# Optimization experiments

Measured on AMD Instinct MI355X. Metric: run time of the kernel, lower is better.

Reference implementation:

```python
import jax, jax.numpy as jnp
import numpy as np

N = 10000          # nodes
E_RAND = 320000    # random edges (avg degree 32)
F_IN = 512         # nfeat
HID = 256          # args.hid
HEADS = 8          # args.head
FH = HID // HEADS  # 32 per head
NCLASS = 40
TAU = 0.5
LAMDA = 0.5
K = 2


def setup_inputs() -> dict:
    key = jax.random.key(0)
    ks = jax.random.split(key, 16)
    # edge list: random edges + self-loops (so every dst segment is non-empty)
    src = jnp.concatenate([jax.random.randint(ks[0], (E_RAND,), 0, N), jnp.arange(N)])
    dst = jnp.concatenate([jax.random.randint(ks[1], (E_RAND,), 0, N), jnp.arange(N)])
    s = 0.05  # small init scale keeps exp() in attention/bind_loss stable
    return {
        "x": jax.random.normal(ks[2], (N, F_IN), jnp.float32),
        "src": src, "dst": dst,
        "W0": jax.random.normal(ks[3], (F_IN, HEADS, FH), jnp.float32) * s,
        "a0s": jax.random.normal(ks[4], (HEADS, FH), jnp.float32) * s,
        "a0d": jax.random.normal(ks[5], (HEADS, FH), jnp.float32) * s,
        "W1": jax.random.normal(ks[6], (HID, HEADS, FH), jnp.float32) * s,
        "a1s": jax.random.normal(ks[7], (HEADS, FH), jnp.float32) * s,
        "a1d": jax.random.normal(ks[8], (HEADS, FH), jnp.float32) * s,
        "W2": jax.random.normal(ks[9], (HID, HEADS, FH), jnp.float32) * s,
        "a2s": jax.random.normal(ks[10], (HEADS, FH), jnp.float32) * s,
        "a2d": jax.random.normal(ks[11], (HEADS, FH), jnp.float32) * s,
        "Wout": jax.random.normal(ks[12], (HID, HEADS, NCLASS), jnp.float32) * s,
        "aos": jax.random.normal(ks[13], (HEADS, NCLASS), jnp.float32) * s,
        "aod": jax.random.normal(ks[14], (HEADS, NCLASS), jnp.float32) * s,
    }


def _gat_layer(x, W, a_s, a_d, src, dst):
    """Sparse multi-head GAT layer: gather -> edge softmax -> scatter."""
    n = x.shape[0]
    h = jnp.einsum('nf,fhd->nhd', x, W)              # [N,H,Fh]
    es = jnp.sum(h * a_s, axis=-1)                    # [N,H]
    ed = jnp.sum(h * a_d, axis=-1)                    # [N,H]
    e = jax.nn.leaky_relu(es[src] + ed[dst], 0.2)     # [E,H]
    m = jax.ops.segment_max(e, dst, num_segments=n)   # per-dst max (stable softmax)
    w = jnp.exp(e - m[dst])
    z = jax.ops.segment_sum(w, dst, num_segments=n)
    alpha = w / z[dst]                                # [E,H]
    return jax.ops.segment_sum(alpha[:, :, None] * h[src], dst, num_segments=n)  # [N,H,Fh]


def _bind_loss(z):
    # z1 == z2 == z in the original call site: refl_sim == between_sim
    zn = z / jnp.maximum(jnp.linalg.norm(z, axis=1, keepdims=True), 1e-12)
    S = jnp.exp(jnp.matmul(zn, zn.T) / TAU)           # [N,N]
    d = jnp.diagonal(S)
    off = jnp.sum(S, axis=1) - d                      # masked (off-diagonal) row sum
    CT = -jnp.log(d / (off + off))                    # neg_c2.sum + neg_c3.sum
    return jnp.mean(CT)


def reference(x, src, dst, W0, a0s, a0d, W1, a1s, a1d, W2, a2s, a2d, Wout, aos, aod):
    layers = [(W0, a0s, a0d), (W1, a1s, a1d), (W2, a2s, a2d)]
    last = x
    loss = jnp.float32(0.0)
    for i, (W, as_, ad_) in enumerate(layers):
        cur = jax.nn.elu(_gat_layer(last, W, as_, ad_, src, dst))
        cur = cur.reshape(cur.shape[0], -1)           # concat heads -> [N, HID]
        if i > 0:
            beta = LAMDA / (i + 2)                    # MaskLayer(last, cur, lamda, i+2)
            cur = beta * last + (1.0 - beta) * cur
            if i % K == 0:
                loss = loss + _bind_loss(cur)
        last = cur
    out = _gat_layer(last, Wout, aos, aod, src, dst).mean(axis=1)  # avg heads -> [N,C]
    return (jax.nn.log_softmax(out, axis=1), loss)
```

## Files before the change

kernel.cpp:

```cpp
#include <hip/hip_runtime.h>
#include <hip/hip_bf16.h>
#include <math.h>

#define NN_F_IN   512
#define NN_HID    256
#define NN_HEADS  8
#define NN_FH     32
#define NN_NCLASS 40
#define TAU_F     0.5f
#define LAMDA_F   0.5f
#define ZN_SCALE  1.6986436f

typedef __attribute__((ext_vector_type(8))) short bf16x8;
typedef __attribute__((ext_vector_type(4))) float f32x4;

typedef __attribute__((address_space(1))) unsigned int gu32_t;
typedef __attribute__((address_space(3))) unsigned int lu32_t;

static __device__ __forceinline__ float lrelu02(float x) { return x >= 0.f ? x : 0.2f * x; }
static __device__ __forceinline__ float elu1(float x)    { return x > 0.f ? x : expm1f(x); }
static __device__ __forceinline__ float b2f(unsigned short u) {
    unsigned int x = ((unsigned int)u) << 16;
    return __uint_as_float(x);
}
static __device__ __forceinline__ unsigned short f2b(float f) {
    __hip_bfloat16 hb = __float2bfloat16(f);
    return *reinterpret_cast<unsigned short*>(&hb);
}

__global__ void prep_kernel(const float* __restrict__ x,
                            const float* __restrict__ W0, const float* __restrict__ W1,
                            const float* __restrict__ W2, const float* __restrict__ Wo,
                            unsigned short* __restrict__ Xb,
                            unsigned short* __restrict__ Wt0, unsigned short* __restrict__ Wt1,
                            unsigned short* __restrict__ Wt2, unsigned short* __restrict__ Wto,
                            int n4X) {
    int i = blockIdx.x * 256 + threadIdx.x;
    if (i < n4X) {
        float4 v = *(const float4*)(x + (size_t)i * 4);
        ushort4 o;
        o.x = f2b(v.x); o.y = f2b(v.y); o.z = f2b(v.z); o.w = f2b(v.w);
        *(ushort4*)(Xb + (size_t)i * 4) = o;
        return;
    }
    i -= n4X;
    if (i < 256 * 512) {
        int np = i >> 9, k = i & 511;
        Wt0[i] = f2b(W0[(size_t)k * 256 + np]);
        return;
    }
    i -= 256 * 512;
    if (i < 256 * 256) {
        int np = i >> 8, k = i & 255;
        Wt1[i] = f2b(W1[(size_t)k * 256 + np]);
        return;
    }
    i -= 256 * 256;
    if (i < 256 * 256) {
        int np = i >> 8, k = i & 255;
        Wt2[i] = f2b(W2[(size_t)k * 256 + np]);
        return;
    }
    i -= 256 * 256;
    if (i < 384 * 256) {
        int np = i >> 8, k = i & 255;
        Wto[i] = f2b(np < 320 ? Wo[(size_t)k * 320 + np] : 0.f);
    }
}

__global__ __launch_bounds__(256) void fc_mfma(const unsigned short* __restrict__ A,
                                               const unsigned short* __restrict__ B,
                                               unsigned short* __restrict__ H,
                                               int M, int K, int ncols, int ldH) {
    int t = threadIdx.x, lane = t & 63, wid = t >> 6;
    int wrow = wid >> 1, wcol = wid & 1;
    int l15 = lane & 15, lg = lane >> 4;
    int mbase = blockIdx.y * 64 + wrow * 32;
    int nbase = blockIdx.x * 64 + wcol * 32;

    const unsigned short* Ap[2];
    const unsigned short* Bp[2];
#pragma unroll
    for (int m = 0; m < 2; ++m) {
        int rr = mbase + m * 16 + l15;
        if (rr > M - 1) rr = M - 1;
        Ap[m] = A + (size_t)rr * K + lg * 8;
        Bp[m] = B + (size_t)(nbase + m * 16 + l15) * K + lg * 8;
    }
    f32x4 acc[2][2];
#pragma unroll
    for (int m = 0; m < 2; ++m)
#pragma unroll
        for (int nn = 0; nn < 2; ++nn)
#pragma unroll
            for (int r = 0; r < 4; ++r) acc[m][nn][r] = 0.f;

    bf16x8 aP[2], bP[2], aQ[2], bQ[2];
#pragma unroll
    for (int m = 0; m < 2; ++m) {
        aP[m] = *(const bf16x8*)(Ap[m]);
        bP[m] = *(const bf16x8*)(Bp[m]);
    }
    int nhalf = K >> 6;
    int kk = 32;
    for (int it = 0; it < nhalf; ++it) {
#pragma unroll
        for (int m = 0; m < 2; ++m) {
            aQ[m] = *(const bf16x8*)(Ap[m] + kk);
            bQ[m] = *(const bf16x8*)(Bp[m] + kk);
        }
#pragma unroll
        for (int m = 0; m < 2; ++m)
#pragma unroll
            for (int nn = 0; nn < 2; ++nn)
                acc[m][nn] = __builtin_amdgcn_mfma_f32_16x16x32_bf16(aP[m], bP[nn], acc[m][nn], 0, 0, 0);
        if (it + 1 < nhalf) {
#pragma unroll
            for (int m = 0; m < 2; ++m) {
                aP[m] = *(const bf16x8*)(Ap[m] + kk + 32);
                bP[m] = *(const bf16x8*)(Bp[m] + kk + 32);
            }
        }
#pragma unroll
        for (int m = 0; m < 2; ++m)
#pragma unroll
            for (int nn = 0; nn < 2; ++nn)
                acc[m][nn] = __builtin_amdgcn_mfma_f32_16x16x32_bf16(aQ[m], bQ[nn], acc[m][nn], 0, 0, 0);
        kk += 64;
    }
#pragma unroll
    for (int m = 0; m < 2; ++m) {
#pragma unroll
        for (int nn = 0; nn < 2; ++nn) {
            int col = nbase + nn * 16 + l15;
            if (col >= ncols) continue;
#pragma unroll
            for (int r = 0; r < 4; ++r) {
                int row = mbase + m * 16 + lg * 4 + r;
                if (row < M) H[(size_t)row * ldH + col] = f2b(acc[m][nn][r]);
            }
        }
    }
}

__global__ void attn_kernel(const unsigned short* __restrict__ Hm, const float* __restrict__ As,
                            const float* __restrict__ Ad, float* __restrict__ es,
                            float* __restrict__ ed, int n, int df) {
    int idx = blockIdx.x * blockDim.x + threadIdx.x;
    if (idx >= n * NN_HEADS) return;
    int nn = idx / NN_HEADS, hh = idx - nn * NN_HEADS;
    const unsigned short* hp = Hm + (size_t)nn * NN_HEADS * df + hh * df;
    const float* ap = As + hh * df;
    const float* bp = Ad + hh * df;
    float s1 = 0.f, s2 = 0.f;
    for (int d = 0; d < df; d += 4) {
        ushort4 hv = *(const ushort4*)(hp + d);
        float4 av = *(const float4*)(ap + d);
        float4 bv = *(const float4*)(bp + d);
        float h0 = b2f(hv.x), h1 = b2f(hv.y), h2 = b2f(hv.z), h3 = b2f(hv.w);
        s1 += h0 * av.x + h1 * av.y + h2 * av.z + h3 * av.w;
        s2 += h0 * bv.x + h1 * bv.y + h2 * bv.z + h3 * bv.w;
    }
    es[idx] = s1;
    ed[idx] = s2;
}

__global__ __launch_bounds__(256) void edge_wz(
    const float* __restrict__ es, const float* __restrict__ ed,
    const int* __restrict__ csr_src, const int* __restrict__ row_start,
    float* __restrict__ wC, float* __restrict__ zinv, int n) {
    int lane = threadIdx.x & 63;
    int nn   = blockIdx.x * 4 + (threadIdx.x >> 6);
    if (nn >= n) return;
    int s0 = row_start[nn], s1 = row_start[nn + 1];
    int h    = lane & 7;
    int slot = lane >> 3;
    float edh = ed[nn * NN_HEADS + h];
    float z = 0.f;
    for (int e = s0 + slot; e < s1; e += 8) {
        int sv = csr_src[e];
        float w = __expf(lrelu02(es[sv * NN_HEADS + h] + edh));
        wC[(size_t)e * NN_HEADS + h] = w;
        z += w;
    }
    z += __shfl_xor(z, 8, 64);
    z += __shfl_xor(z, 16, 64);
    z += __shfl_xor(z, 32, 64);
    if (slot == 0) zinv[nn * NN_HEADS + h] = 1.f / z;
}

__global__ void count_kernel(const int* __restrict__ dst, int* __restrict__ counts, int E) {
    int e = blockIdx.x * blockDim.x + threadIdx.x;
    if (e < E) atomicAdd(&counts[dst[e]], 1);
}

__global__ void scan_kernel(const int* __restrict__ counts, int* __restrict__ row_start,
                            int* __restrict__ cursor, int n) {
    __shared__ int s[1024];
    int t  = threadIdx.x;
    int ch = (n + 1023) / 1024;
    int lo = t * ch;
    int sum = 0;
    for (int j = 0; j < ch; ++j) {
        int i = lo + j;
        if (i < n) sum += counts[i];
    }
    s[t] = sum;
    __syncthreads();
    for (int off = 1; off < 1024; off <<= 1) {
        int v = 0;
        if (t >= off) v = s[t - off];
        __syncthreads();
        s[t] += v;
        __syncthreads();
    }
    int run = (t == 0) ? 0 : s[t - 1];
    for (int j = 0; j < ch; ++j) {
        int i = lo + j;
        if (i < n) {
            row_start[i] = run;
            cursor[i] = run;
            run += counts[i];
        }
    }
    if (t == 1023) row_start[n] = s[1023];
}

__global__ void scatter_kernel(const int* __restrict__ src, const int* __restrict__ dst,
                               int* __restrict__ cursor, int* __restrict__ csr_src, int E) {
    int e = blockIdx.x * blockDim.x + threadIdx.x;
    if (e < E) {
        int d   = dst[e];
        int pos = atomicAdd(&cursor[d], 1);
        csr_src[pos] = src[e];
    }
}

__global__ __launch_bounds__(256) void gather_hidden(
    const unsigned short* __restrict__ Hm, const float* __restrict__ es,
    const float* __restrict__ ed, const int* __restrict__ csr_src,
    const int* __restrict__ row_start, const unsigned short* __restrict__ last,
    unsigned short* __restrict__ out, int n, float beta) {
    int lane = threadIdx.x & 63;
    int nn   = blockIdx.x * 4 + (threadIdx.x >> 6);
    if (nn >= n) return;
    int s0 = row_start[nn], s1 = row_start[nn + 1];
    int h2 = lane >> 3;
    float edh = ed[nn * NN_HEADS + h2];

    float zacc = 0.f;
    float a0 = 0.f, a1 = 0.f, a2 = 0.f, a3 = 0.f;
    int fullEnd = s0 + ((s1 - s0) & ~7);
    int e = s0;
    for (; e < fullEnd; e += 8) {
        int idx[8];
        float q[8];
#pragma unroll
        for (int j = 0; j < 8; ++j) idx[j] = csr_src[e + j];
#pragma unroll
        for (int j = 0; j < 8; ++j) q[j] = es[idx[j] * NN_HEADS + h2];
        ushort4 r[8];
#pragma unroll
        for (int j = 0; j < 8; ++j) r[j] = *(const ushort4*)&Hm[(size_t)idx[j] * NN_HID + lane * 4];
#pragma unroll
        for (int j = 0; j < 8; ++j) {
            float w = __expf(lrelu02(q[j] + edh));
            zacc += w;
            a0 += w * b2f(r[j].x); a1 += w * b2f(r[j].y);
            a2 += w * b2f(r[j].z); a3 += w * b2f(r[j].w);
        }
    }
    if (e < s1) {
        int c = s1 - e;
        int idx[8];
        float q[8];
#pragma unroll
        for (int j = 0; j < 8; ++j) idx[j] = csr_src[(j < c) ? e + j : e];
#pragma unroll
        for (int j = 0; j < 8; ++j) q[j] = es[idx[j] * NN_HEADS + h2];
        ushort4 r[8];
#pragma unroll
        for (int j = 0; j < 8; ++j) r[j] = *(const ushort4*)&Hm[(size_t)idx[j] * NN_HID + lane * 4];
#pragma unroll
        for (int j = 0; j < 8; ++j) {
            if (j < c) {
                float w = __expf(lrelu02(q[j] + edh));
                zacc += w;
                a0 += w * b2f(r[j].x); a1 += w * b2f(r[j].y);
                a2 += w * b2f(r[j].z); a3 += w * b2f(r[j].w);
            }
        }
    }
    float zi = 1.f / zacc;
    float v0 = elu1(a0 * zi), v1 = elu1(a1 * zi), v2 = elu1(a2 * zi), v3 = elu1(a3 * zi);
    if (beta >= 0.f) {
        ushort4 lv = *(const ushort4*)&last[(size_t)nn * NN_HID + lane * 4];
        v0 = beta * b2f(lv.x) + (1.f - beta) * v0;
        v1 = beta * b2f(lv.y) + (1.f - beta) * v1;
        v2 = beta * b2f(lv.z) + (1.f - beta) * v2;
        v3 = beta * b2f(lv.w) + (1.f - beta) * v3;
    }
    ushort4 o;
    o.x = f2b(v0); o.y = f2b(v1); o.z = f2b(v2); o.w = f2b(v3);
    *(ushort4*)&out[(size_t)nn * NN_HID + lane * 4] = o;
}

__global__ void gather_final(const unsigned short* __restrict__ Hm, const float* __restrict__ wC,
                             const float* __restrict__ zinv, const int* __restrict__ csr_src,
                             const int* __restrict__ row_start, float* __restrict__ dout, int n) {
    int nn = blockIdx.x;
    __shared__ float accs[NN_HEADS * NN_NCLASS];
    int t = threadIdx.x;
    int s0 = row_start[nn], s1 = row_start[nn + 1];
    int hh = t / NN_NCLASS;
    float acc = 0.f;
    const int LD = NN_HEADS * NN_NCLASS;
    int fullEnd = s0 + ((s1 - s0) & ~7);
    int e = s0;
    for (; e < fullEnd; e += 8) {
        int idx[8];
        float wv[8];
#pragma unroll
        for (int j = 0; j < 8; ++j) {
            idx[j] = csr_src[e + j];
            wv[j]  = wC[(size_t)(e + j) * NN_HEADS + hh];
        }
        float v[8];
#pragma unroll
        for (int j = 0; j < 8; ++j) v[j] = b2f(Hm[(size_t)idx[j] * LD + t]);
#pragma unroll
        for (int j = 0; j < 8; ++j) acc += wv[j] * v[j];
    }
    if (e < s1) {
        int c = s1 - e;
        int idx[8];
        float wv[8];
#pragma unroll
        for (int j = 0; j < 8; ++j) {
            int p = (j < c) ? e + j : e;
            idx[j] = csr_src[p];
            wv[j]  = wC[(size_t)p * NN_HEADS + hh];
        }
        float v[8];
#pragma unroll
        for (int j = 0; j < 8; ++j) v[j] = b2f(Hm[(size_t)idx[j] * LD + t]);
#pragma unroll
        for (int j = 0; j < 8; ++j) {
            if (j < c) acc += wv[j] * v[j];
        }
    }
    accs[t] = acc * zinv[nn * NN_HEADS + hh];
    __syncthreads();
    if (t < 64) {
        float v = -INFINITY;
        if (t < NN_NCLASS) {
            float sacc = 0.f;
#pragma unroll
            for (int h2 = 0; h2 < NN_HEADS; ++h2) sacc += accs[h2 * NN_NCLASS + t];
            v = sacc * (1.f / NN_HEADS);
        }
        float mx = v;
#pragma unroll
        for (int o = 1; o < 64; o <<= 1) mx = fmaxf(mx, __shfl_xor(mx, o, 64));
        float ex = (t < NN_NCLASS) ? expf(v - mx) : 0.f;
        float se = ex;
#pragma unroll
        for (int o = 1; o < 64; o <<= 1) se += __shfl_xor(se, o, 64);
        if (t < NN_NCLASS) dout[(size_t)nn * NN_NCLASS + t] = (v - mx) - logf(se);
    }
}

__global__ void rownorm_kernel(const unsigned short* __restrict__ z, short* __restrict__ znb,
                               float* __restrict__ dvec, int n) {
    int nn = blockIdx.x;
    int t  = threadIdx.x;
    if (nn >= n) {
        znb[(size_t)nn * NN_HID + t] = 0;
        return;
    }
    float v  = b2f(z[(size_t)nn * NN_HID + t]);
    float sq = v * v;
#pragma unroll
    for (int o = 1; o < 64; o <<= 1) sq += __shfl_xor(sq, o, 64);
    __shared__ float ws[4];
    if ((t & 63) == 0) ws[t >> 6] = sq;
    __syncthreads();
    float s = ws[0] + ws[1] + ws[2] + ws[3];
    float m = fmaxf(sqrtf(s), 1e-12f);
    znb[(size_t)nn * NN_HID + t] = (short)f2b((v / m) * ZN_SCALE);
    if (t == 0) dvec[nn] = __expf((s / (m * m)) * (1.f / TAU_F));
}

__global__ __launch_bounds__(256) void gram_mfma(const short* __restrict__ znb,
                                                 float* __restrict__ P2d, int n,
                                                 int T, int nwg, int Npad) {
    __shared__ short As[128 * 32];
    __shared__ short Bs[128 * 32];

    int b = blockIdx.x;
    int q = nwg >> 3, r8 = nwg & 7, xc = b & 7, oo = b >> 3;
    int sid = (xc < r8 ? xc * (q + 1) : r8 * (q + 1) + (xc - r8) * q) + oo;
    int bi = 0, rem = sid;
    while (rem >= T - bi) { rem -= T - bi; ++bi; }
    int bj = bi + rem;
    int i0 = bi * 128, j0 = bj * 128;

    int t    = threadIdx.x;
    int lane = t & 63;
    int wid  = t >> 6;
    int wrow = wid >> 1, wcol = wid & 1;
    int l15  = lane & 15, lg = lane >> 4;

    int srow0 = 16 * (2 * wid + 0) + (lane >> 2);
    int srow1 = 16 * (2 * wid + 1) + (lane >> 2);
    int kc    = lane & 3;
    int kc0   = kc ^ ((srow0 >> 1) & 3);
    int kc1   = kc ^ ((srow1 >> 1) & 3);
    const short* gA0 = znb + (size_t)(i0 + srow0) * NN_HID + kc0 * 8;
    const short* gA1 = znb + (size_t)(i0 + srow1) * NN_HID + kc1 * 8;
    const short* gB0 = znb + (size_t)(j0 + srow0) * NN_HID + kc0 * 8;
    const short* gB1 = znb + (size_t)(j0 + srow1) * NN_HID + kc1 * 8;
    short* lA0 = As + (2 * wid + 0) * 512 + lane * 8;
    short* lA1 = As + (2 * wid + 1) * 512 + lane * 8;
    short* lB0 = Bs + (2 * wid + 0) * 512 + lane * 8;
    short* lB1 = Bs + (2 * wid + 1) * 512 + lane * 8;

    f32x4 acc[4][4];
#pragma unroll
    for (int m = 0; m < 4; ++m)
#pragma unroll
        for (int nn = 0; nn < 4; ++nn)
#pragma unroll
            for (int r = 0; r < 4; ++r) acc[m][nn][r] = 0.f;

#pragma unroll
    for (int s = 0; s < 8; ++s) {
        int ko = s * 32;
        __builtin_amdgcn_global_load_lds((gu32_t*)(gA0 + ko), (lu32_t*)lA0, 16, 0, 0);
        __builtin_amdgcn_global_load_lds((gu32_t*)(gA1 + ko), (lu32_t*)lA1, 16, 0, 0);
        __builtin_amdgcn_global_load_lds((gu32_t*)(gB0 + ko), (lu32_t*)lB0, 16, 0, 0);
        __builtin_amdgcn_global_load_lds((gu32_t*)(gB1 + ko), (lu32_t*)lB1, 16, 0, 0);
        __syncthreads();
        bf16x8 av[4], bv[4];
#pragma unroll
        for (int m = 0; m < 4; ++m) {
            int Ra = wrow * 64 + m * 16 + l15;
            int ca = lg ^ ((Ra >> 1) & 3);
            av[m] = *(const bf16x8*)&As[Ra * 32 + ca * 8];
        }
#pragma unroll
        for (int m = 0; m < 4; ++m) {
            int Rb = wcol * 64 + m * 16 + l15;
            int cb = lg ^ ((Rb >> 1) & 3);
            bv[m] = *(const bf16x8*)&Bs[Rb * 32 + cb * 8];
        }
#pragma unroll
        for (int m = 0; m < 4; ++m)
#pragma unroll
            for (int nn = 0; nn < 4; ++nn)
                acc[m][nn] = __builtin_amdgcn_mfma_f32_16x16x32_bf16(av[m], bv[nn], acc[m][nn], 0, 0, 0);
        __syncthreads();
    }

    int i0w = i0 + wrow * 64;
    int j0w = j0 + wcol * 64;
    bool diag = (bj == bi);
    if (bj == T - 1) {
#pragma unroll
        for (int m = 0; m < 4; ++m)
#pragma unroll
            for (int nn = 0; nn < 4; ++nn) {
                int gj = j0w + nn * 16 + l15;
                bool jok = gj < n;
#pragma unroll
                for (int r = 0; r < 4; ++r) {
                    int gi = i0w + m * 16 + lg * 4 + r;
                    acc[m][nn][r] = (jok && gi < n) ? __builtin_exp2f(acc[m][nn][r]) : 0.f;
                }
            }
    } else {
#pragma unroll
        for (int m = 0; m < 4; ++m)
#pragma unroll
            for (int nn = 0; nn < 4; ++nn)
#pragma unroll
                for (int r = 0; r < 4; ++r)
                    acc[m][nn][r] = __builtin_exp2f(acc[m][nn][r]);
    }
    float* rowslot = P2d + (size_t)(2 * bj + wcol) * Npad;
#pragma unroll
    for (int m = 0; m < 4; ++m) {
#pragma unroll
        for (int r = 0; r < 4; ++r) {
            float v = acc[m][0][r] + acc[m][1][r] + acc[m][2][r] + acc[m][3][r];
            v += __shfl_xor(v, 1, 64);
            v += __shfl_xor(v, 2, 64);
            v += __shfl_xor(v, 4, 64);
            v += __shfl_xor(v, 8, 64);
            if (l15 == 0) {
                int gi = i0w + m * 16 + lg * 4 + r;
                if (gi < n) rowslot[gi] = v;
            }
        }
    }
    if (!diag) {
        float* colslot = P2d + (size_t)(2 * bi + wrow) * Npad;
#pragma unroll
        for (int nn = 0; nn < 4; ++nn) {
            float v = 0.f;
#pragma unroll
            for (int m = 0; m < 4; ++m)
#pragma unroll
                for (int r = 0; r < 4; ++r) v += acc[m][nn][r];
            v += __shfl_xor(v, 16, 64);
            v += __shfl_xor(v, 32, 64);
            if (lg == 0) {
                int gj = j0w + nn * 16 + l15;
                if (gj < n) colslot[gj] = v;
            }
        }
    }
}

__global__ void fold_kernel(const float* __restrict__ P2d, float* __restrict__ R,
                            int n, int slots, int Npad) {
    int i = blockIdx.x * 256 + threadIdx.x;
    if (i >= n) return;
    const float* p = P2d + i;
    float s0 = 0.f, s1 = 0.f, s2 = 0.f, s3 = 0.f;
    int sl = 0;
    for (; sl + 4 <= slots; sl += 4) {
        s0 += p[(size_t)(sl + 0) * Npad];
        s1 += p[(size_t)(sl + 1) * Npad];
        s2 += p[(size_t)(sl + 2) * Npad];
        s3 += p[(size_t)(sl + 3) * Npad];
    }
    for (; sl < slots; ++sl) s0 += p[(size_t)sl * Npad];
    R[i] = (s0 + s1) + (s2 + s3);
}

__global__ void loss_kernel(const float* __restrict__ R, const float* __restrict__ dvec,
                            float* __restrict__ out_loss, int n) {
    __shared__ float s[1024];
    int t = threadIdx.x;
    float sum = 0.f;
    for (int i = t; i < n; i += 1024) {
        float d   = dvec[i];
        float off = R[i] - d;
        sum += -logf(d / (off + off));
    }
    s[t] = sum;
    __syncthreads();
    for (int o = 512; o > 0; o >>= 1) {
        if (t < o) s[t] += s[t + o];
        __syncthreads();
    }
    if (t == 0) *out_loss = s[0] / n;
}

extern "C" void kernel_launch(void* const* d_in, const int* in_sizes, int n_in,
                              void* d_out, int out_size, void* d_ws, size_t ws_size,
                              hipStream_t stream) {
    const float* x   = (const float*)d_in[0];
    const int*   src = (const int*)d_in[1];
    const int*   dst = (const int*)d_in[2];
    const float* W0  = (const float*)d_in[3];
    const float* a0s = (const float*)d_in[4];
    const float* a0d = (const float*)d_in[5];
    const float* W1  = (const float*)d_in[6];
    const float* a1s = (const float*)d_in[7];
    const float* a1d = (const float*)d_in[8];
    const float* W2  = (const float*)d_in[9];
    const float* a2s = (const float*)d_in[10];
    const float* a2d = (const float*)d_in[11];
    const float* Wout= (const float*)d_in[12];
    const float* aos = (const float*)d_in[13];
    const float* aod = (const float*)d_in[14];

    int N = in_sizes[0] / NN_F_IN;
    int E = in_sizes[1];
    int Npad = ((N + 127) / 128) * 128;
    int T = Npad / 128;
    int nwg = T * (T + 1) / 2;
    float* out = (float*)d_out;

    char*  ws  = (char*)d_ws;
    size_t off = 0;
    auto alloc = [&](size_t bytes) -> void* {
        void* p = ws + off;
        off += bytes;
        off = (off + 255) & ~(size_t)255;
        return p;
    };
    size_t hbBytes = (size_t)N * 320 * 2;
    size_t znBytes = (size_t)Npad * NN_HID * 2;
    unsigned short* Hb = (unsigned short*)alloc(hbBytes > znBytes ? hbBytes : znBytes);
    short* znb = (short*)Hb;
    unsigned short* Bl = (unsigned short*)alloc((size_t)N * NN_HID * 2);
    unsigned short* Bc = (unsigned short*)alloc((size_t)N * NN_HID * 2);
    size_t xbBytes = (size_t)N * NN_F_IN * 2;
    size_t p2Bytes = (size_t)2 * T * Npad * 4;
    void* XbP2d = alloc(xbBytes > p2Bytes ? xbBytes : p2Bytes);
    unsigned short* Xb  = (unsigned short*)XbP2d;
    float*          P2d = (float*)XbP2d;
    unsigned short* Wt0 = (unsigned short*)alloc((size_t)256 * 512 * 2);
    unsigned short* Wt1 = (unsigned short*)alloc((size_t)256 * 256 * 2);
    unsigned short* Wt2 = (unsigned short*)alloc((size_t)256 * 256 * 2);
    unsigned short* Wto = (unsigned short*)alloc((size_t)384 * 256 * 2);
    float* es     = (float*)alloc((size_t)N * NN_HEADS * 4);
    float* ed     = (float*)alloc((size_t)N * NN_HEADS * 4);
    float* wC     = (float*)alloc((size_t)E * NN_HEADS * 4);
    float* zinvA  = (float*)alloc((size_t)N * NN_HEADS * 4);
    float* Rrow   = (float*)alloc((size_t)N * 4);
    float* dvec   = (float*)alloc((size_t)N * 4);
    int*   counts = (int*)alloc((size_t)N * 4);
    int*   rs     = (int*)alloc((size_t)(N + 1) * 4);
    int*   cursor = (int*)alloc((size_t)N * 4);
    int*   csr    = (int*)alloc((size_t)E * 4);

    hipMemsetAsync(counts, 0, (size_t)N * 4, stream);
    count_kernel<<<(E + 255) / 256, 256, 0, stream>>>(dst, counts, E);
    scan_kernel<<<1, 1024, 0, stream>>>(counts, rs, cursor, N);
    scatter_kernel<<<(E + 255) / 256, 256, 0, stream>>>(src, dst, cursor, csr, E);

    int n4X = N * NN_F_IN / 4;
    int prepTotal = n4X + 256 * 512 + 256 * 256 + 256 * 256 + 384 * 256;
    prep_kernel<<<(prepTotal + 255) / 256, 256, 0, stream>>>(
        x, W0, W1, W2, Wout, Xb, Wt0, Wt1, Wt2, Wto, n4X);

    int atGrid = (N * NN_HEADS + 255) / 256;
    int ghGrid = (N + 3) / 4;
    int mT64 = (N + 63) / 64;

    fc_mfma<<<dim3(4, mT64), 256, 0, stream>>>(Xb, Wt0, Hb, N, 512, 256, 256);
    attn_kernel<<<atGrid, 256, 0, stream>>>(Hb, a0s, a0d, es, ed, N, NN_FH);
    gather_hidden<<<ghGrid, 256, 0, stream>>>(Hb, es, ed, csr, rs, nullptr, Bl, N, -1.f);

    fc_mfma<<<dim3(4, mT64), 256, 0, stream>>>(Bl, Wt1, Hb, N, 256, 256, 256);
    attn_kernel<<<atGrid, 256, 0, stream>>>(Hb, a1s, a1d, es, ed, N, NN_FH);
    gather_hidden<<<ghGrid, 256, 0, stream>>>(Hb, es, ed, csr, rs, Bl, Bc, N, LAMDA_F / 3.f);

    fc_mfma<<<dim3(4, mT64), 256, 0, stream>>>(Bc, Wt2, Hb, N, 256, 256, 256);
    attn_kernel<<<atGrid, 256, 0, stream>>>(Hb, a2s, a2d, es, ed, N, NN_FH);
    gather_hidden<<<ghGrid, 256, 0, stream>>>(Hb, es, ed, csr, rs, Bc, Bl, N, LAMDA_F / 4.f);

    rownorm_kernel<<<Npad, 256, 0, stream>>>(Bl, znb, dvec, N);
    gram_mfma<<<nwg, 256, 0, stream>>>(znb, P2d, N, T, nwg, Npad);
    fold_kernel<<<(N + 255) / 256, 256, 0, stream>>>(P2d, Rrow, N, 2 * T, Npad);
    loss_kernel<<<1, 1024, 0, stream>>>(Rrow, dvec, out + (size_t)N * NN_NCLASS, N);

    fc_mfma<<<dim3(5, mT64), 256, 0, stream>>>(Bl, Wto, Hb, N, 256, 320, 320);
    attn_kernel<<<atGrid, 256, 0, stream>>>(Hb, aos, aod, es, ed, N, NN_NCLASS);
    edge_wz<<<ghGrid, 256, 0, stream>>>(es, ed, csr, rs, wC, zinvA, N);
    gather_final<<<N, NN_HEADS * NN_NCLASS, 0, stream>>>(Hb, wC, zinvA, csr, rs, out, N);
}
```

Measured before the change: 384.8 us.

## Fuse attention scores into FC GEMM, row-norm into gather, double-buffer gram

Computes the per-head es/ed attention logits inside the FC MFMA epilogue using shuffles across the 32 columns of each head, which removes the three separate attn kernels for the hidden layers. The row normalisation for the contrastive loss moves into the last gather_hidden, removing the rownorm kernel, so znb gets its own buffer and its padding rows are zeroed by a memset. The gram kernel double-buffers its LDS tiles so the global-to-LDS load of the next K slice overlaps the MFMAs on the current one. The cost is extra LDS use and a separate znb allocation. The normalisation is now computed from fp32 values before bf16 rounding, so results can differ slightly.

```diff
diff --git a/kernel.cpp b/kernel.cpp
--- a/kernel.cpp
+++ b/kernel.cpp
@@ -65,6 +65,104 @@
     if (i < 384 * 256) {
         int np = i >> 8, k = i & 255;
         Wto[i] = f2b(np < 320 ? Wo[(size_t)k * 320 + np] : 0.f);
+    }
+}
+
+__global__ __launch_bounds__(256) void fc_attn_mfma(
+    const unsigned short* __restrict__ A, const unsigned short* __restrict__ B,
+    unsigned short* __restrict__ H, const float* __restrict__ As_,
+    const float* __restrict__ Ad_, float* __restrict__ es, float* __restrict__ ed,
+    int M, int K) {
+    const int ldH = 256;
+    int t = threadIdx.x, lane = t & 63, wid = t >> 6;
+    int wrow = wid >> 1, wcol = wid & 1;
+    int l15 = lane & 15, lg = lane >> 4;
+    int mbase = blockIdx.y * 64 + wrow * 32;
+    int nbase = blockIdx.x * 64 + wcol * 32;
+
+    const unsigned short* Ap[2];
+    const unsigned short* Bp[2];
+#pragma unroll
+    for (int m = 0; m < 2; ++m) {
+        int rr = mbase + m * 16 + l15;
+        if (rr > M - 1) rr = M - 1;
+        Ap[m] = A + (size_t)rr * K + lg * 8;
+        Bp[m] = B + (size_t)(nbase + m * 16 + l15) * K + lg * 8;
+    }
+    f32x4 acc[2][2];
+#pragma unroll
+    for (int m = 0; m < 2; ++m)
+#pragma unroll
+        for (int nn = 0; nn < 2; ++nn)
+#pragma unroll
+            for (int r = 0; r < 4; ++r) acc[m][nn][r] = 0.f;
+
+    bf16x8 aP[2], bP[2], aQ[2], bQ[2];
+#pragma unroll
+    for (int m = 0; m < 2; ++m) {
+        aP[m] = *(const bf16x8*)(Ap[m]);
+        bP[m] = *(const bf16x8*)(Bp[m]);
+    }
+    int nhalf = K >> 6;
+    int kk = 32;
+    for (int it = 0; it < nhalf; ++it) {
+#pragma unroll
+        for (int m = 0; m < 2; ++m) {
+            aQ[m] = *(const bf16x8*)(Ap[m] + kk);
+            bQ[m] = *(const bf16x8*)(Bp[m] + kk);
+        }
+#pragma unroll
+        for (int m = 0; m < 2; ++m)
+#pragma unroll
+            for (int nn = 0; nn < 2; ++nn)
+                acc[m][nn] = __builtin_amdgcn_mfma_f32_16x16x32_bf16(aP[m], bP[nn], acc[m][nn], 0, 0, 0);
+        if (it + 1 < nhalf) {
+#pragma unroll
+            for (int m = 0; m < 2; ++m) {
+                aP[m] = *(const bf16x8*)(Ap[m] + kk + 32);
+                bP[m] = *(const bf16x8*)(Bp[m] + kk + 32);
+            }
+        }
+#pragma unroll
+        for (int m = 0; m < 2; ++m)
+#pragma unroll
+            for (int nn = 0; nn < 2; ++nn)
+                acc[m][nn] = __builtin_amdgcn_mfma_f32_16x16x32_bf16(aQ[m], bQ[nn], acc[m][nn], 0, 0, 0);
+        kk += 64;
+    }
+#pragma unroll
+    for (int m = 0; m < 2; ++m) {
+#pragma unroll
+        for (int nn = 0; nn < 2; ++nn) {
+            int col = nbase + nn * 16 + l15;
+#pragma unroll
+            for (int r = 0; r < 4; ++r) {
+                int row = mbase + m * 16 + lg * 4 + r;
+                if (row < M) H[(size_t)row * ldH + col] = f2b(acc[m][nn][r]);
+            }
+        }
+    }
+    int hh = blockIdx.x * 2 + wcol;
+    float a0 = As_[hh * 32 + l15], a1 = As_[hh * 32 + 16 + l15];
+    float d0 = Ad_[hh * 32 + l15], d1 = Ad_[hh * 32 + 16 + l15];
+#pragma unroll
+    for (int m = 0; m < 2; ++m) {
+#pragma unroll
+        for (int r = 0; r < 4; ++r) {
+            float ps = acc[m][0][r] * a0 + acc[m][1][r] * a1;
+            float pd = acc[m][0][r] * d0 + acc[m][1][r] * d1;
+            ps += __shfl_xor(ps, 1, 64); pd += __shfl_xor(pd, 1, 64);
+            ps += __shfl_xor(ps, 2, 64); pd += __shfl_xor(pd, 2, 64);
+            ps += __shfl_xor(ps, 4, 64); pd += __shfl_xor(pd, 4, 64);
+            ps += __shfl_xor(ps, 8, 64); pd += __shfl_xor(pd, 8, 64);
+            if (l15 == 0) {
+                int row = mbase + m * 16 + lg * 4 + r;
+                if (row < M) {
+                    es[row * NN_HEADS + hh] = ps;
+                    ed[row * NN_HEADS + hh] = pd;
+                }
+            }
+        }
     }
 }
 
@@ -240,7 +338,8 @@
     const unsigned short* __restrict__ Hm, const float* __restrict__ es,
     const float* __restrict__ ed, const int* __restrict__ csr_src,
     const int* __restrict__ row_start, const unsigned short* __restrict__ last,
-    unsigned short* __restrict__ out, int n, float beta) {
+    unsigned short* __restrict__ out, int n, float beta,
+    unsigned short* __restrict__ znb, float* __restrict__ dvec) {
     int lane = threadIdx.x & 63;
     int nn   = blockIdx.x * 4 + (threadIdx.x >> 6);
     if (nn >= n) return;
@@ -303,6 +402,23 @@
     ushort4 o;
     o.x = f2b(v0); o.y = f2b(v1); o.z = f2b(v2); o.w = f2b(v3);
     *(ushort4*)&out[(size_t)nn * NN_HID + lane * 4] = o;
+
+    if (znb) {
+        float ss = v0 * v0 + v1 * v1 + v2 * v2 + v3 * v3;
+        ss += __shfl_xor(ss, 1, 64);
+        ss += __shfl_xor(ss, 2, 64);
+        ss += __shfl_xor(ss, 4, 64);
+        ss += __shfl_xor(ss, 8, 64);
+        ss += __shfl_xor(ss, 16, 64);
+        ss += __shfl_xor(ss, 32, 64);
+        float m = fmaxf(sqrtf(ss), 1e-12f);
+        float sc = ZN_SCALE / m;
+        ushort4 zo;
+        zo.x = f2b(v0 * sc); zo.y = f2b(v1 * sc);
+        zo.z = f2b(v2 * sc); zo.w = f2b(v3 * sc);
+        *(ushort4*)&znb[(size_t)nn * NN_HID + lane * 4] = zo;
+        if (lane == 0) dvec[nn] = __expf((ss / (m * m)) * (1.f / TAU_F));
+    }
 }
 
 __global__ void gather_final(const unsigned short* __restrict__ Hm, const float* __restrict__ wC,
@@ -370,32 +486,11 @@
     }
 }
 
-__global__ void rownorm_kernel(const unsigned short* __restrict__ z, short* __restrict__ znb,
-                               float* __restrict__ dvec, int n) {
-    int nn = blockIdx.x;
-    int t  = threadIdx.x;
-    if (nn >= n) {
-        znb[(size_t)nn * NN_HID + t] = 0;
-        return;
-    }
-    float v  = b2f(z[(size_t)nn * NN_HID + t]);
-    float sq = v * v;
-#pragma unroll
-    for (int o = 1; o < 64; o <<= 1) sq += __shfl_xor(sq, o, 64);
-    __shared__ float ws[4];
-    if ((t & 63) == 0) ws[t >> 6] = sq;
-    __syncthreads();
-    float s = ws[0] + ws[1] + ws[2] + ws[3];
-    float m = fmaxf(sqrtf(s), 1e-12f);
-    znb[(size_t)nn * NN_HID + t] = (short)f2b((v / m) * ZN_SCALE);
-    if (t == 0) dvec[nn] = __expf((s / (m * m)) * (1.f / TAU_F));
-}
-
 __global__ __launch_bounds__(256) void gram_mfma(const short* __restrict__ znb,
                                                  float* __restrict__ P2d, int n,
                                                  int T, int nwg, int Npad) {
-    __shared__ short As[128 * 32];
-    __shared__ short Bs[128 * 32];
+    __shared__ short As[2][128 * 32];
+    __shared__ short Bs[2][128 * 32];
 
     int b = blockIdx.x;
     int q = nwg >> 3, r8 = nwg & 7, xc = b & 7, oo = b >> 3;
@@ -420,10 +515,16 @@
     const short* gA1 = znb + (size_t)(i0 + srow1) * NN_HID + kc1 * 8;
     const short* gB0 = znb + (size_t)(j0 + srow0) * NN_HID + kc0 * 8;
     const short* gB1 = znb + (size_t)(j0 + srow1) * NN_HID + kc1 * 8;
-    short* lA0 = As + (2 * wid + 0) * 512 + lane * 8;
-    short* lA1 = As + (2 * wid + 1) * 512 + lane * 8;
-    short* lB0 = Bs + (2 * wid + 0) * 512 + lane * 8;
-    short* lB1 = Bs + (2 * wid + 1) * 512 + lane * 8;
+    int ldst0 = (2 * wid + 0) * 512 + lane * 8;
+    int ldst1 = (2 * wid + 1) * 512 + lane * 8;
+
+    auto stage = [&](int buf, int s) {
+        int ko = s * 32;
+        __builtin_amdgcn_global_load_lds((gu32_t*)(gA0 + ko), (lu32_t*)(&As[buf][ldst0]), 16, 0, 0);
+        __builtin_amdgcn_global_load_lds((gu32_t*)(gA1 + ko), (lu32_t*)(&As[buf][ldst1]), 16, 0, 0);
+        __builtin_amdgcn_global_load_lds((gu32_t*)(gB0 + ko), (lu32_t*)(&Bs[buf][ldst0]), 16, 0, 0);
+        __builtin_amdgcn_global_load_lds((gu32_t*)(gB1 + ko), (lu32_t*)(&Bs[buf][ldst1]), 16, 0, 0);
+    };
 
     f32x4 acc[4][4];
 #pragma unroll
@@ -433,26 +534,24 @@
 #pragma unroll
             for (int r = 0; r < 4; ++r) acc[m][nn][r] = 0.f;
 
+    stage(0, 0);
+    __syncthreads();
 #pragma unroll
     for (int s = 0; s < 8; ++s) {
-        int ko = s * 32;
-        __builtin_amdgcn_global_load_lds((gu32_t*)(gA0 + ko), (lu32_t*)lA0, 16, 0, 0);
-        __builtin_amdgcn_global_load_lds((gu32_t*)(gA1 + ko), (lu32_t*)lA1, 16, 0, 0);
-        __builtin_amdgcn_global_load_lds((gu32_t*)(gB0 + ko), (lu32_t*)lB0, 16, 0, 0);
-        __builtin_amdgcn_global_load_lds((gu32_t*)(gB1 + ko), (lu32_t*)lB1, 16, 0, 0);
-        __syncthreads();
+        int cur = s & 1;
+        if (s < 7) stage(cur ^ 1, s + 1);
         bf16x8 av[4], bv[4];
 #pragma unroll
         for (int m = 0; m < 4; ++m) {
             int Ra = wrow * 64 + m * 16 + l15;
             int ca = lg ^ ((Ra >> 1) & 3);
-            av[m] = *(const bf16x8*)&As[Ra * 32 + ca * 8];
+            av[m] = *(const bf16x8*)&As[cur][Ra * 32 + ca * 8];
         }
 #pragma unroll
         for (int m = 0; m < 4; ++m) {
             int Rb = wcol * 64 + m * 16 + l15;
             int cb = lg ^ ((Rb >> 1) & 3);
-            bv[m] = *(const bf16x8*)&Bs[Rb * 32 + cb * 8];
+            bv[m] = *(const bf16x8*)&Bs[cur][Rb * 32 + cb * 8];
         }
 #pragma unroll
         for (int m = 0; m < 4; ++m)
@@ -592,10 +691,8 @@
         off = (off + 255) & ~(size_t)255;
         return p;
     };
-    size_t hbBytes = (size_t)N * 320 * 2;
-    size_t znBytes = (size_t)Npad * NN_HID * 2;
-    unsigned short* Hb = (unsigned short*)alloc(hbBytes > znBytes ? hbBytes : znBytes);
-    short* znb = (short*)Hb;
+    unsigned short* Hb = (unsigned short*)alloc((size_t)N * 320 * 2);
+    unsigned short* znb = (unsigned short*)alloc((size_t)Npad * NN_HID * 2);
     unsigned short* Bl = (unsigned short*)alloc((size_t)N * NN_HID * 2);
     unsigned short* Bc = (unsigned short*)alloc((size_t)N * NN_HID * 2);
     size_t xbBytes = (size_t)N * NN_F_IN * 2;
@@ -619,6 +716,8 @@
     int*   csr    = (int*)alloc((size_t)E * 4);
 
     hipMemsetAsync(counts, 0, (size_t)N * 4, stream);
+    if (Npad > N)
+        hipMemsetAsync(znb + (size_t)N * NN_HID, 0, (size_t)(Npad - N) * NN_HID * 2, stream);
     count_kernel<<<(E + 255) / 256, 256, 0, stream>>>(dst, counts, E);
     scan_kernel<<<1, 1024, 0, stream>>>(counts, rs, cursor, N);
     scatter_kernel<<<(E + 255) / 256, 256, 0, stream>>>(src, dst, cursor, csr, E);
@@ -632,20 +731,19 @@
     int ghGrid = (N + 3) / 4;
     int mT64 = (N + 63) / 64;
 
-    fc_mfma<<<dim3(4, mT64), 256, 0, stream>>>(Xb, Wt0, Hb, N, 512, 256, 256);
-    attn_kernel<<<atGrid, 256, 0, stream>>>(Hb, a0s, a0d, es, ed, N, NN_FH);
-    gather_hidden<<<ghGrid, 256, 0, stream>>>(Hb, es, ed, csr, rs, nullptr, Bl, N, -1.f);
-
-    fc_mfma<<<dim3(4, mT64), 256, 0, stream>>>(Bl, Wt1, Hb, N, 256, 256, 256);
-    attn_kernel<<<atGrid, 256, 0, stream>>>(Hb, a1s, a1d, es, ed, N, NN_FH);
-    gather_hidden<<<ghGrid, 256, 0, stream>>>(Hb, es, ed, csr, rs, Bl, Bc, N, LAMDA_F / 3.f);
-
-    fc_mfma<<<dim3(4, mT64), 256, 0, stream>>>(Bc, Wt2, Hb, N, 256, 256, 256);
-    attn_kernel<<<atGrid, 256, 0, stream>>>(Hb, a2s, a2d, es, ed, N, NN_FH);
-    gather_hidden<<<ghGrid, 256, 0, stream>>>(Hb, es, ed, csr, rs, Bc, Bl, N, LAMDA_F / 4.f);
-
-    rownorm_kernel<<<Npad, 256, 0, stream>>>(Bl, znb, dvec, N);
-    gram_mfma<<<nwg, 256, 0, stream>>>(znb, P2d, N, T, nwg, Npad);
+    fc_attn_mfma<<<dim3(4, mT64), 256, 0, stream>>>(Xb, Wt0, Hb, a0s, a0d, es, ed, N, 512);
+    gather_hidden<<<ghGrid, 256, 0, stream>>>(Hb, es, ed, csr, rs, nullptr, Bl, N, -1.f,
+                                              nullptr, nullptr);
+
+    fc_attn_mfma<<<dim3(4, mT64), 256, 0, stream>>>(Bl, Wt1, Hb, a1s, a1d, es, ed, N, 256);
+    gather_hidden<<<ghGrid, 256, 0, stream>>>(Hb, es, ed, csr, rs, Bl, Bc, N, LAMDA_F / 3.f,
+                                              nullptr, nullptr);
+
+    fc_attn_mfma<<<dim3(4, mT64), 256, 0, stream>>>(Bc, Wt2, Hb, a2s, a2d, es, ed, N, 256);
+    gather_hidden<<<ghGrid, 256, 0, stream>>>(Hb, es, ed, csr, rs, Bc, Bl, N, LAMDA_F / 4.f,
+                                              znb, dvec);
+
+    gram_mfma<<<nwg, 256, 0, stream>>>((const short*)znb, P2d, N, T, nwg, Npad);
     fold_kernel<<<(N + 255) / 256, 256, 0, stream>>>(P2d, Rrow, N, 2 * T, Npad);
     loss_kernel<<<1, 1024, 0, stream>>>(Rrow, dvec, out + (size_t)N * NN_NCLASS, N);
 
```

After: 366.9 us. -4.7%, faster.
